# Optimization experiments

Hardware: AMD Instinct MI355X
Metric: run time of the kernel (lower is better)

## Reference

```python
import jax, jax.numpy as jnp
import numpy as np

N = 50000      # num nodes
NE = 20000     # num hyperedges
NNZ = 1000000  # incidence pairs |{(v,e)}|
F_IN = 128
HID = 64
NCLS = 40
NLAYER = 4
ALPHA = 0.1    # args.restart_alpha
LAMDA = 0.5


def setup_inputs() -> dict:
    key = jax.random.key(0)
    ks = jax.random.split(key, 8)
    x = jax.random.normal(ks[0], (N, F_IN), dtype=jnp.float32)
    vertex = jax.random.randint(ks[1], (NNZ,), 0, N, dtype=jnp.int32)
    edges = jax.random.randint(ks[2], (NNZ,), 0, NE, dtype=jnp.int32)
    W0 = jax.random.normal(ks[3], (F_IN, HID), dtype=jnp.float32) / np.float32(np.sqrt(F_IN))
    b0 = jnp.zeros((HID,), jnp.float32)
    Ws = jax.random.normal(ks[4], (NLAYER, HID, HID), dtype=jnp.float32) / np.float32(np.sqrt(HID))
    Wout = jax.random.normal(ks[5], (HID, NCLS), dtype=jnp.float32) / np.float32(np.sqrt(HID))
    bout = jnp.zeros((NCLS,), jnp.float32)
    return {"x": x, "vertex": vertex, "edges": edges, "W0": W0, "b0": b0,
            "Ws": Ws, "Wout": Wout, "bout": bout}


def _scatter_mean(src, idx, num_segments):
    s = jax.ops.segment_sum(src, idx, num_segments=num_segments)
    cnt = jax.ops.segment_sum(jnp.ones((idx.shape[0],), src.dtype), idx, num_segments=num_segments)
    return s / jnp.maximum(cnt, 1.0)[:, None]


def _normalize_l2(X):
    # torch: rownorm = X.detach().norm(dim=1, keepdim=True); scale = rownorm^-1; inf->0
    norm = jax.lax.stop_gradient(jnp.sqrt(jnp.sum(X * X, axis=-1, keepdims=True)))
    scale = jnp.where(norm > 0, 1.0 / jnp.maximum(norm, jnp.float32(1e-30)), 0.0)
    return X * scale


def reference(x, vertex, edges, W0, b0, Ws, Wout, bout):
    # input linear + relu (dropout = identity in eval mode)
    X = jax.nn.relu(x @ W0 + b0)
    X0 = X
    for i in range(NLAYER):
        beta = float(np.log(LAMDA / (i + 1) + 1.0))
        Xve = X[vertex]                       # gather node -> incidence  [NNZ, HID]
        Xe = _scatter_mean(Xve, edges, NE)    # scatter-mean -> hyperedge [NE, HID]
        Xev = Xe[edges]                       # gather hyperedge -> incidence [NNZ, HID]
        Xv = _scatter_mean(Xev, vertex, N)    # scatter-mean -> node      [N, HID]
        Xv = _normalize_l2(Xv)                # args.UniGNN_use_norm = True
        Xi = (1.0 - ALPHA) * Xv + ALPHA * X0
        X = jax.nn.relu((1.0 - beta) * Xi + beta * (Xi @ Ws[i]))
    return X @ Wout + bout
```

## Files before the change

### kernel.cpp

```cpp
#include <hip/hip_runtime.h>
#include <hip/hip_fp16.h>
#include <math.h>

#define N_NODES 50000
#define N_EDGES 20000
#define NNZ_C   1000000
#define F_IN    128
#define HID     64
#define NCLS    40
#define NLAYER  4
#define ALPHA   0.1f

#define ESHIFT  6
#define VSHIFT  7
#define NB_E    ((N_EDGES + 63) / 64)
#define NB_V    ((N_NODES + 127) / 128)
#define NB_TOT  (NB_E + NB_V)
#define MAXNB   391

typedef _Float16 f16x8 __attribute__((ext_vector_type(8)));
typedef float    f32x4 __attribute__((ext_vector_type(4)));

__global__ __launch_bounds__(256) void input_gemm(
    const float* __restrict__ x, const float* __restrict__ W0,
    const float* __restrict__ b0, _Float16* __restrict__ X0h,
    _Float16* __restrict__ Xh)
{
    int lane = threadIdx.x & 63;
    int wv   = threadIdx.x >> 6;
    int r16  = lane & 15;
    int kgrp = lane >> 4;
    f16x8 bf[4][4];
    #pragma unroll
    for (int n0 = 0; n0 < 4; ++n0)
        #pragma unroll
        for (int kh = 0; kh < 4; ++kh)
            #pragma unroll
            for (int j = 0; j < 8; ++j)
                bf[n0][kh][j] = (_Float16)W0[(kh * 32 + kgrp * 8 + j) * HID + n0 * 16 + r16];
    float bias[4];
    #pragma unroll
    for (int n0 = 0; n0 < 4; ++n0) bias[n0] = b0[n0 * 16 + r16];

    int nwaves = gridDim.x * 4;
    for (int t = blockIdx.x * 4 + wv; t < N_NODES / 16; t += nwaves) {
        int row0 = t * 16;
        const float* xp = x + (size_t)(row0 + r16) * F_IN + kgrp * 8;
        f16x8 a[4];
        #pragma unroll
        for (int kh = 0; kh < 4; ++kh) {
            float4 u0 = *(const float4*)(xp + kh * 32);
            float4 u1 = *(const float4*)(xp + kh * 32 + 4);
            a[kh][0] = (_Float16)u0.x; a[kh][1] = (_Float16)u0.y;
            a[kh][2] = (_Float16)u0.z; a[kh][3] = (_Float16)u0.w;
            a[kh][4] = (_Float16)u1.x; a[kh][5] = (_Float16)u1.y;
            a[kh][6] = (_Float16)u1.z; a[kh][7] = (_Float16)u1.w;
        }
        #pragma unroll
        for (int n0 = 0; n0 < 4; ++n0) {
            f32x4 acc = {0.f, 0.f, 0.f, 0.f};
            #pragma unroll
            for (int kh = 0; kh < 4; ++kh)
                acc = __builtin_amdgcn_mfma_f32_16x16x32_f16(a[kh], bf[n0][kh], acc, 0, 0, 0);
            #pragma unroll
            for (int r = 0; r < 4; ++r) {
                float y = acc[r] + bias[n0];
                y = y > 0.f ? y : 0.f;
                _Float16 h = (_Float16)y;
                size_t o = (size_t)(row0 + kgrp * 4 + r) * HID + n0 * 16 + r16;
                X0h[o] = h;
                Xh[o]  = h;
            }
        }
    }
}

__global__ __launch_bounds__(256) void make_wp(
    const float* __restrict__ Ws, _Float16* __restrict__ Wp,
    float be0, float be1, float be2, float be3)
{
    int l = blockIdx.x;
    float beta = (l == 0) ? be0 : (l == 1) ? be1 : (l == 2) ? be2 : be3;
    for (int i = threadIdx.x; i < HID * HID; i += 256) {
        int k = i >> 6, n = i & 63;
        float v = beta * Ws[l * HID * HID + i] + ((k == n) ? (1.f - beta) : 0.f);
        Wp[l * HID * HID + i] = (_Float16)v;
    }
}

__global__ __launch_bounds__(256) void bucket_hist(
    const int* __restrict__ vertex, const int* __restrict__ edges,
    int* __restrict__ gcnt)
{
    __shared__ int h[NB_TOT];
    int tid = threadIdx.x;
    for (int i = tid; i < NB_TOT; i += 256) h[i] = 0;
    __syncthreads();
    int base = blockIdx.x * 4096;
    int n = NNZ_C - base; if (n > 4096) n = 4096;
    for (int i = tid * 4; i < n; i += 1024) {
        int4 e4 = *(const int4*)(edges  + base + i);
        int4 v4 = *(const int4*)(vertex + base + i);
        atomicAdd(&h[e4.x >> ESHIFT], 1);
        atomicAdd(&h[e4.y >> ESHIFT], 1);
        atomicAdd(&h[e4.z >> ESHIFT], 1);
        atomicAdd(&h[e4.w >> ESHIFT], 1);
        atomicAdd(&h[NB_E + (v4.x >> VSHIFT)], 1);
        atomicAdd(&h[NB_E + (v4.y >> VSHIFT)], 1);
        atomicAdd(&h[NB_E + (v4.z >> VSHIFT)], 1);
        atomicAdd(&h[NB_E + (v4.w >> VSHIFT)], 1);
    }
    __syncthreads();
    for (int i = tid; i < NB_TOT; i += 256)
        if (h[i]) atomicAdd(&gcnt[i], h[i]);
}

__global__ __launch_bounds__(1024) void bucket_scan(
    const int* __restrict__ gcnt, int* __restrict__ boff_e,
    int* __restrict__ boff_v, int* __restrict__ curb)
{
    __shared__ int tmp[1024];
    int tid = threadIdx.x;
    int v = (tid < NB_TOT) ? gcnt[tid] : 0;
    tmp[tid] = v;
    __syncthreads();
    for (int d = 1; d < 1024; d <<= 1) {
        int t = (tid >= d) ? tmp[tid - d] : 0;
        __syncthreads();
        tmp[tid] += t;
        __syncthreads();
    }
    if (tid < NB_TOT) {
        int excl = tmp[tid] - v;
        int off = (tid < NB_E) ? excl : excl - NNZ_C;
        if (tid < NB_E) boff_e[tid] = off; else boff_v[tid - NB_E] = off;
        curb[tid] = off;
    }
    if (tid == 0) { boff_e[NB_E] = NNZ_C; boff_v[NB_V] = NNZ_C; }
}

__global__ __launch_bounds__(256) void bin_pass1(
    const int* __restrict__ keys, const int* __restrict__ vals,
    int shift, int nb, int* __restrict__ cur,
    unsigned long long* __restrict__ binned)
{
    __shared__ int hist[MAXNB];
    __shared__ int base[MAXNB];
    int tid = threadIdx.x;
    int blk = blockIdx.x * 4096;
    int nh = NNZ_C - blk; if (nh > 4096) nh = 4096;
    for (int i = tid; i < nb; i += 256) hist[i] = 0;
    __syncthreads();
    for (int i = tid; i < nh; i += 256)
        atomicAdd(&hist[keys[blk + i] >> shift], 1);
    __syncthreads();
    for (int i = tid; i < nb; i += 256) {
        int c = hist[i];
        base[i] = c ? atomicAdd(&cur[i], c) : 0;
        hist[i] = 0;
    }
    __syncthreads();
    for (int i = tid; i < nh; i += 256) {
        int k = keys[blk + i], v = vals[blk + i];
        int bkt = k >> shift;
        int r = atomicAdd(&hist[bkt], 1);
        binned[base[bkt] + r] = ((unsigned long long)(unsigned)k << 32) | (unsigned)v;
    }
}

__global__ __launch_bounds__(256) void bin_pass2f(
    const unsigned long long* __restrict__ binned, const int* __restrict__ boff,
    int shift, int nkeys, int* __restrict__ off, float* __restrict__ inv,
    int* __restrict__ adj)
{
    __shared__ int lcnt[128];
    __shared__ int ts[128];
    __shared__ int lcur[128];
    int b  = blockIdx.x;
    int k0 = b << shift;
    int bs = 1 << shift;
    int kn = nkeys - k0; if (kn > bs) kn = bs;
    int tid = threadIdx.x;
    if (tid < 128) lcnt[tid] = 0;
    __syncthreads();
    int beg = boff[b], end = boff[b + 1];
    for (int j = beg + tid; j < end; j += 256)
        atomicAdd(&lcnt[(int)(binned[j] >> 32) - k0], 1);
    __syncthreads();
    int c = 0;
    if (tid < 128) { c = lcnt[tid]; ts[tid] = c; }
    __syncthreads();
    #pragma unroll
    for (int d = 1; d < 128; d <<= 1) {
        int t = 0;
        if (tid < 128 && tid >= d) t = ts[tid - d];
        __syncthreads();
        if (tid < 128) ts[tid] += t;
        __syncthreads();
    }
    if (tid < kn) {
        int pos = beg + ts[tid] - c;
        off[k0 + tid] = pos;
        inv[k0 + tid] = 1.0f / fmaxf((float)c, 1.0f);
        lcur[tid] = pos;
    }
    if (b == 0 && tid == 0) off[nkeys] = NNZ_C;
    __syncthreads();
    for (int j = beg + tid; j < end; j += 256) {
        unsigned long long p = binned[j];
        int k = (int)(p >> 32) - k0;
        int v = (int)(p & 0xffffffffULL);
        adj[atomicAdd(&lcur[k], 1)] = v;
    }
}

__device__ __forceinline__ void gather_rows(
    const __half* __restrict__ src, const int* __restrict__ adj,
    int beg, int end, int lane, float acc[8])
{
    int g = lane >> 3, c = lane & 7;
    for (int j = beg; j < end; j += 64) {
        int nj = end - j; if (nj > 64) nj = 64;
        int myidx = (lane < nj) ? adj[j + lane] : 0;
        for (int s = 0; (s << 3) < nj; ++s) {
            int r = (s << 3) + g;
            int srcl = r < nj ? r : 0;
            int idx = __shfl(myidx, srcl);
            if (r < nj) {
                uint4 raw = ((const uint4*)(src + (size_t)idx * HID))[c];
                union { uint4 u; __half2 h[4]; } U; U.u = raw;
                float2 f0 = __half22float2(U.h[0]);
                float2 f1 = __half22float2(U.h[1]);
                float2 f2 = __half22float2(U.h[2]);
                float2 f3 = __half22float2(U.h[3]);
                acc[0] += f0.x; acc[1] += f0.y;
                acc[2] += f1.x; acc[3] += f1.y;
                acc[4] += f2.x; acc[5] += f2.y;
                acc[6] += f3.x; acc[7] += f3.y;
            }
        }
    }
    #pragma unroll
    for (int q = 0; q < 8; ++q) {
        acc[q] += __shfl_xor(acc[q], 8);
        acc[q] += __shfl_xor(acc[q], 16);
        acc[q] += __shfl_xor(acc[q], 32);
    }
}

__global__ __launch_bounds__(256) void edge_gather(
    const __half* __restrict__ Xh, const int* __restrict__ adj_e,
    const int* __restrict__ off_e, const float* __restrict__ inv_e,
    __half* __restrict__ Xeh)
{
    int wid  = blockIdx.x * 4 + (threadIdx.x >> 6);
    int lane = threadIdx.x & 63;
    float acc[8] = {0.f,0.f,0.f,0.f,0.f,0.f,0.f,0.f};
    gather_rows(Xh, adj_e, off_e[wid], off_e[wid + 1], lane, acc);
    if ((lane >> 3) == 0) {
        float sc = inv_e[wid];
        union { uint4 u; __half2 h[4]; } O;
        O.h[0] = __floats2half2_rn(acc[0] * sc, acc[1] * sc);
        O.h[1] = __floats2half2_rn(acc[2] * sc, acc[3] * sc);
        O.h[2] = __floats2half2_rn(acc[4] * sc, acc[5] * sc);
        O.h[3] = __floats2half2_rn(acc[6] * sc, acc[7] * sc);
        ((uint4*)(Xeh + (size_t)wid * HID))[lane] = O.u;
    }
}

__global__ __launch_bounds__(256) void node_gather(
    const __half* __restrict__ Xeh, const int* __restrict__ adj_v,
    const int* __restrict__ off_v, const float* __restrict__ inv_v,
    const _Float16* __restrict__ X0h, _Float16* __restrict__ Xi)
{
    int wv   = threadIdx.x >> 6;
    int row  = blockIdx.x * 4 + wv;
    int lane = threadIdx.x & 63;
    float acc[8] = {0.f,0.f,0.f,0.f,0.f,0.f,0.f,0.f};
    gather_rows(Xeh, adj_v, off_v[row], off_v[row + 1], lane, acc);
    float scm = inv_v[row];
    float m[8]; float s = 0.f;
    #pragma unroll
    for (int q = 0; q < 8; ++q) { m[q] = acc[q] * scm; s += m[q] * m[q]; }
    s += __shfl_xor(s, 1);
    s += __shfl_xor(s, 2);
    s += __shfl_xor(s, 4);
    float norm  = sqrtf(s);
    float scale = norm > 0.f ? 1.0f / norm : 0.f;
    if ((lane >> 3) == 0) {
        union { f16x8 v; uint4 u; } I;
        I.u = *(const uint4*)(X0h + (size_t)row * HID + lane * 8);
        union { f16x8 v; uint4 u; } O;
        #pragma unroll
        for (int q = 0; q < 8; ++q)
            O.v[q] = (_Float16)((1.0f - ALPHA) * (m[q] * scale) + ALPHA * (float)I.v[q]);
        *(uint4*)(Xi + (size_t)row * HID + lane * 8) = O.u;
    }
}

__global__ __launch_bounds__(256) void layer_gemm(
    const _Float16* __restrict__ Xi, const _Float16* __restrict__ Wp,
    _Float16* __restrict__ Xh)
{
    int lane = threadIdx.x & 63;
    int wv   = threadIdx.x >> 6;
    int r16  = lane & 15;
    int kgrp = lane >> 4;
    f16x8 bf[4][2];
    #pragma unroll
    for (int n0 = 0; n0 < 4; ++n0)
        #pragma unroll
        for (int kh = 0; kh < 2; ++kh) {
            #pragma unroll
            for (int j = 0; j < 8; ++j)
                bf[n0][kh][j] = Wp[(kh * 32 + kgrp * 8 + j) * HID + n0 * 16 + r16];
        }
    int nwaves = gridDim.x * 4;
    for (int t = blockIdx.x * 4 + wv; t < N_NODES / 16; t += nwaves) {
        int row0 = t * 16;
        const _Float16* ap = Xi + (size_t)(row0 + r16) * HID + kgrp * 8;
        f16x8 a0 = *(const f16x8*)(ap);
        f16x8 a1 = *(const f16x8*)(ap + 32);
        #pragma unroll
        for (int n0 = 0; n0 < 4; ++n0) {
            f32x4 acc = {0.f, 0.f, 0.f, 0.f};
            acc = __builtin_amdgcn_mfma_f32_16x16x32_f16(a0, bf[n0][0], acc, 0, 0, 0);
            acc = __builtin_amdgcn_mfma_f32_16x16x32_f16(a1, bf[n0][1], acc, 0, 0, 0);
            #pragma unroll
            for (int r = 0; r < 4; ++r) {
                float y = acc[r] > 0.f ? acc[r] : 0.f;
                Xh[(size_t)(row0 + kgrp * 4 + r) * HID + n0 * 16 + r16] = (_Float16)y;
            }
        }
    }
}

__global__ __launch_bounds__(256) void out_gemm(
    const _Float16* __restrict__ Xh, const float* __restrict__ Wout,
    const float* __restrict__ bout, float* __restrict__ out)
{
    int lane = threadIdx.x & 63;
    int wv   = threadIdx.x >> 6;
    int r16  = lane & 15;
    int kgrp = lane >> 4;
    f16x8 bf[3][2];
    float bias[3];
    #pragma unroll
    for (int n0 = 0; n0 < 3; ++n0) {
        int col = n0 * 16 + r16;
        bias[n0] = (col < NCLS) ? bout[col] : 0.f;
        #pragma unroll
        for (int kh = 0; kh < 2; ++kh)
            #pragma unroll
            for (int j = 0; j < 8; ++j) {
                int k = kh * 32 + kgrp * 8 + j;
                bf[n0][kh][j] = (col < NCLS) ? (_Float16)Wout[k * NCLS + col] : (_Float16)0.f;
            }
    }
    int nwaves = gridDim.x * 4;
    for (int t = blockIdx.x * 4 + wv; t < N_NODES / 16; t += nwaves) {
        int row0 = t * 16;
        const _Float16* ap = Xh + (size_t)(row0 + r16) * HID + kgrp * 8;
        f16x8 a0 = *(const f16x8*)(ap);
        f16x8 a1 = *(const f16x8*)(ap + 32);
        #pragma unroll
        for (int n0 = 0; n0 < 3; ++n0) {
            f32x4 acc = {0.f, 0.f, 0.f, 0.f};
            acc = __builtin_amdgcn_mfma_f32_16x16x32_f16(a0, bf[n0][0], acc, 0, 0, 0);
            acc = __builtin_amdgcn_mfma_f32_16x16x32_f16(a1, bf[n0][1], acc, 0, 0, 0);
            int col = n0 * 16 + r16;
            if (col < NCLS) {
                #pragma unroll
                for (int r = 0; r < 4; ++r)
                    out[(size_t)(row0 + kgrp * 4 + r) * NCLS + col] = acc[r] + bias[n0];
            }
        }
    }
}

extern "C" void kernel_launch(void* const* d_in, const int* in_sizes, int n_in,
                              void* d_out, int out_size, void* d_ws, size_t ws_size,
                              hipStream_t stream)
{
    const float* x      = (const float*)d_in[0];
    const int*   vertex = (const int*)  d_in[1];
    const int*   edges  = (const int*)  d_in[2];
    const float* W0     = (const float*)d_in[3];
    const float* b0     = (const float*)d_in[4];
    const float* Ws     = (const float*)d_in[5];
    const float* Wout   = (const float*)d_in[6];
    const float* bout   = (const float*)d_in[7];
    float* out = (float*)d_out;

    char* ws = (char*)d_ws;
    unsigned long long* binned = (unsigned long long*)ws; ws += (size_t)NNZ_C * 8;
    _Float16*  X0h  = (_Float16*)ws;  ws += (size_t)N_NODES * HID * 2;
    _Float16*  Xh   = (_Float16*)ws;  ws += (size_t)N_NODES * HID * 2;
    _Float16*  Xi   = (_Float16*)ws;  ws += (size_t)N_NODES * HID * 2;
    __half*    Xeh  = (__half*)ws;    ws += (size_t)N_EDGES * HID * 2;
    _Float16*  Wp   = (_Float16*)ws;  ws += (size_t)NLAYER * HID * HID * 2;
    int*   adj_e  = (int*)ws;     ws += (size_t)NNZ_C * 4;
    int*   adj_v  = (int*)ws;     ws += (size_t)NNZ_C * 4;
    int*   off_e  = (int*)ws;     ws += (size_t)(N_EDGES + 1) * 4;
    int*   off_v  = (int*)ws;     ws += (size_t)(N_NODES + 1) * 4;
    float* inv_e  = (float*)ws;   ws += (size_t)N_EDGES * 4;
    float* inv_v  = (float*)ws;   ws += (size_t)N_NODES * 4;
    int*   gcnt   = (int*)ws;     ws += (size_t)NB_TOT * 4;
    int*   boff_e = (int*)ws;     ws += (size_t)(NB_E + 1) * 4;
    int*   boff_v = (int*)ws;     ws += (size_t)(NB_V + 1) * 4;
    int*   curb   = (int*)ws;     ws += (size_t)NB_TOT * 4;

    const int p1_grid = (NNZ_C + 4095) / 4096;

    hipMemsetAsync(gcnt, 0, (size_t)NB_TOT * 4, stream);
    bucket_hist<<<p1_grid, 256, 0, stream>>>(vertex, edges, gcnt);
    bucket_scan<<<1, 1024, 0, stream>>>(gcnt, boff_e, boff_v, curb);

    bin_pass1<<<p1_grid, 256, 0, stream>>>(edges, vertex, ESHIFT, NB_E, curb, binned);
    bin_pass2f<<<NB_E, 256, 0, stream>>>(binned, boff_e, ESHIFT, N_EDGES, off_e, inv_e, adj_e);
    bin_pass1<<<p1_grid, 256, 0, stream>>>(vertex, edges, VSHIFT, NB_V, curb + NB_E, binned);
    bin_pass2f<<<NB_V, 256, 0, stream>>>(binned, boff_v, VSHIFT, N_NODES, off_v, inv_v, adj_v);

    float be0 = logf(0.5f / 1.f + 1.0f);
    float be1 = logf(0.5f / 2.f + 1.0f);
    float be2 = logf(0.5f / 3.f + 1.0f);
    float be3 = logf(0.5f / 4.f + 1.0f);
    make_wp<<<NLAYER, 256, 0, stream>>>(Ws, Wp, be0, be1, be2, be3);

    input_gemm<<<391, 256, 0, stream>>>(x, W0, b0, X0h, Xh);

    for (int l = 0; l < NLAYER; ++l) {
        edge_gather<<<N_EDGES / 4, 256, 0, stream>>>((__half*)Xh, adj_e, off_e, inv_e, Xeh);
        node_gather<<<N_NODES / 4, 256, 0, stream>>>(
            Xeh, adj_v, off_v, inv_v, X0h, Xi);
        layer_gemm<<<391, 256, 0, stream>>>(Xi, Wp + (size_t)l * HID * HID, Xh);
    }

    out_gemm<<<391, 256, 0, stream>>>(Xh, Wout, bout, out);
}
```

Baseline: 293.4 us.

## Map one segment per 8-lane group in gathers and fuse both binning passes

The edge and node gather kernels now give each group of 8 lanes its own segment instead of one segment per wavefront. Each group loops up to the wave's maximum degree, loading indices directly with no shuffle broadcast and no cross-group reduction. Edges have about 50 incidences and nodes about 20, so the old mapping left many lanes idle and paid reduction overhead. The two bin_pass1 launches are merged into one kernel that reads vertex/edges once and writes two binned buffers, at the cost of an extra 8 MB of workspace. Degree imbalance within a wave can now cause lanes to sit idle.

```diff
diff --git a/kernel.cpp b/kernel.cpp
--- a/kernel.cpp
+++ b/kernel.cpp
@@ -16,7 +16,6 @@
 #define NB_E    ((N_EDGES + 63) / 64)
 #define NB_V    ((N_NODES + 127) / 128)
 #define NB_TOT  (NB_E + NB_V)
-#define MAXNB   391
 
 typedef _Float16 f16x8 __attribute__((ext_vector_type(8)));
 typedef float    f32x4 __attribute__((ext_vector_type(4)));
@@ -139,32 +138,38 @@
     if (tid == 0) { boff_e[NB_E] = NNZ_C; boff_v[NB_V] = NNZ_C; }
 }
 
-__global__ __launch_bounds__(256) void bin_pass1(
-    const int* __restrict__ keys, const int* __restrict__ vals,
-    int shift, int nb, int* __restrict__ cur,
-    unsigned long long* __restrict__ binned)
-{
-    __shared__ int hist[MAXNB];
-    __shared__ int base[MAXNB];
+__global__ __launch_bounds__(256) void bin_pass1_both(
+    const int* __restrict__ vertex, const int* __restrict__ edges,
+    int* __restrict__ curb,
+    unsigned long long* __restrict__ binned_e,
+    unsigned long long* __restrict__ binned_v)
+{
+    __shared__ int hist[NB_TOT];
+    __shared__ int base[NB_TOT];
     int tid = threadIdx.x;
     int blk = blockIdx.x * 4096;
     int nh = NNZ_C - blk; if (nh > 4096) nh = 4096;
-    for (int i = tid; i < nb; i += 256) hist[i] = 0;
-    __syncthreads();
-    for (int i = tid; i < nh; i += 256)
-        atomicAdd(&hist[keys[blk + i] >> shift], 1);
-    __syncthreads();
-    for (int i = tid; i < nb; i += 256) {
+    for (int i = tid; i < NB_TOT; i += 256) hist[i] = 0;
+    __syncthreads();
+    for (int i = tid; i < nh; i += 256) {
+        atomicAdd(&hist[edges[blk + i] >> ESHIFT], 1);
+        atomicAdd(&hist[NB_E + (vertex[blk + i] >> VSHIFT)], 1);
+    }
+    __syncthreads();
+    for (int i = tid; i < NB_TOT; i += 256) {
         int c = hist[i];
-        base[i] = c ? atomicAdd(&cur[i], c) : 0;
+        base[i] = c ? atomicAdd(&curb[i], c) : 0;
         hist[i] = 0;
     }
     __syncthreads();
     for (int i = tid; i < nh; i += 256) {
-        int k = keys[blk + i], v = vals[blk + i];
-        int bkt = k >> shift;
-        int r = atomicAdd(&hist[bkt], 1);
-        binned[base[bkt] + r] = ((unsigned long long)(unsigned)k << 32) | (unsigned)v;
+        int e = edges[blk + i], v = vertex[blk + i];
+        int be = e >> ESHIFT;
+        int r  = atomicAdd(&hist[be], 1);
+        binned_e[base[be] + r] = ((unsigned long long)(unsigned)e << 32) | (unsigned)v;
+        int bv = NB_E + (v >> VSHIFT);
+        int r2 = atomicAdd(&hist[bv], 1);
+        binned_v[base[bv] + r2] = ((unsigned long long)(unsigned)v << 32) | (unsigned)e;
     }
 }
 
@@ -214,38 +219,34 @@
     }
 }
 
-__device__ __forceinline__ void gather_rows(
+__device__ __forceinline__ void gather_seg8(
     const __half* __restrict__ src, const int* __restrict__ adj,
-    int beg, int end, int lane, float acc[8])
-{
-    int g = lane >> 3, c = lane & 7;
-    for (int j = beg; j < end; j += 64) {
-        int nj = end - j; if (nj > 64) nj = 64;
-        int myidx = (lane < nj) ? adj[j + lane] : 0;
-        for (int s = 0; (s << 3) < nj; ++s) {
-            int r = (s << 3) + g;
-            int srcl = r < nj ? r : 0;
-            int idx = __shfl(myidx, srcl);
-            if (r < nj) {
-                uint4 raw = ((const uint4*)(src + (size_t)idx * HID))[c];
-                union { uint4 u; __half2 h[4]; } U; U.u = raw;
-                float2 f0 = __half22float2(U.h[0]);
-                float2 f1 = __half22float2(U.h[1]);
-                float2 f2 = __half22float2(U.h[2]);
-                float2 f3 = __half22float2(U.h[3]);
-                acc[0] += f0.x; acc[1] += f0.y;
-                acc[2] += f1.x; acc[3] += f1.y;
-                acc[4] += f2.x; acc[5] += f2.y;
-                acc[6] += f3.x; acc[7] += f3.y;
-            }
-        }
-    }
-    #pragma unroll
-    for (int q = 0; q < 8; ++q) {
-        acc[q] += __shfl_xor(acc[q], 8);
-        acc[q] += __shfl_xor(acc[q], 16);
-        acc[q] += __shfl_xor(acc[q], 32);
-    }
+    int beg, int deg, int md, int c, float acc[8])
+{
+    for (int t = 0; t < md; ++t) {
+        if (t < deg) {
+            int idx = adj[beg + t];
+            uint4 raw = ((const uint4*)(src + (size_t)idx * HID))[c];
+            union { uint4 u; __half2 h[4]; } U; U.u = raw;
+            float2 f0 = __half22float2(U.h[0]);
+            float2 f1 = __half22float2(U.h[1]);
+            float2 f2 = __half22float2(U.h[2]);
+            float2 f3 = __half22float2(U.h[3]);
+            acc[0] += f0.x; acc[1] += f0.y;
+            acc[2] += f1.x; acc[3] += f1.y;
+            acc[4] += f2.x; acc[5] += f2.y;
+            acc[6] += f3.x; acc[7] += f3.y;
+        }
+    }
+}
+
+__device__ __forceinline__ int wave_max_deg(int deg)
+{
+    int md = deg;
+    md = max(md, __shfl_xor(md, 8));
+    md = max(md, __shfl_xor(md, 16));
+    md = max(md, __shfl_xor(md, 32));
+    return md;
 }
 
 __global__ __launch_bounds__(256) void edge_gather(
@@ -255,17 +256,20 @@
 {
     int wid  = blockIdx.x * 4 + (threadIdx.x >> 6);
     int lane = threadIdx.x & 63;
+    int g = lane >> 3, c = lane & 7;
+    int e = wid * 8 + g;
+    int beg = off_e[e];
+    int deg = off_e[e + 1] - beg;
+    int md  = wave_max_deg(deg);
     float acc[8] = {0.f,0.f,0.f,0.f,0.f,0.f,0.f,0.f};
-    gather_rows(Xh, adj_e, off_e[wid], off_e[wid + 1], lane, acc);
-    if ((lane >> 3) == 0) {
-        float sc = inv_e[wid];
-        union { uint4 u; __half2 h[4]; } O;
-        O.h[0] = __floats2half2_rn(acc[0] * sc, acc[1] * sc);
-        O.h[1] = __floats2half2_rn(acc[2] * sc, acc[3] * sc);
-        O.h[2] = __floats2half2_rn(acc[4] * sc, acc[5] * sc);
-        O.h[3] = __floats2half2_rn(acc[6] * sc, acc[7] * sc);
-        ((uint4*)(Xeh + (size_t)wid * HID))[lane] = O.u;
-    }
+    gather_seg8(Xh, adj_e, beg, deg, md, c, acc);
+    float sc = inv_e[e];
+    union { uint4 u; __half2 h[4]; } O;
+    O.h[0] = __floats2half2_rn(acc[0] * sc, acc[1] * sc);
+    O.h[1] = __floats2half2_rn(acc[2] * sc, acc[3] * sc);
+    O.h[2] = __floats2half2_rn(acc[4] * sc, acc[5] * sc);
+    O.h[3] = __floats2half2_rn(acc[6] * sc, acc[7] * sc);
+    *(uint4*)(Xeh + (size_t)e * HID + c * 8) = O.u;
 }
 
 __global__ __launch_bounds__(256) void node_gather(
@@ -273,28 +277,33 @@
     const int* __restrict__ off_v, const float* __restrict__ inv_v,
     const _Float16* __restrict__ X0h, _Float16* __restrict__ Xi)
 {
-    int wv   = threadIdx.x >> 6;
-    int row  = blockIdx.x * 4 + wv;
+    int wid  = blockIdx.x * 4 + (threadIdx.x >> 6);
     int lane = threadIdx.x & 63;
+    int g = lane >> 3, c = lane & 7;
+    int v = wid * 8 + g;
+    bool ok = v < N_NODES;
+    int beg = 0, deg = 0;
+    if (ok) { beg = off_v[v]; deg = off_v[v + 1] - beg; }
+    int md = wave_max_deg(deg);
     float acc[8] = {0.f,0.f,0.f,0.f,0.f,0.f,0.f,0.f};
-    gather_rows(Xeh, adj_v, off_v[row], off_v[row + 1], lane, acc);
-    float scm = inv_v[row];
-    float m[8]; float s = 0.f;
-    #pragma unroll
-    for (int q = 0; q < 8; ++q) { m[q] = acc[q] * scm; s += m[q] * m[q]; }
-    s += __shfl_xor(s, 1);
-    s += __shfl_xor(s, 2);
-    s += __shfl_xor(s, 4);
-    float norm  = sqrtf(s);
-    float scale = norm > 0.f ? 1.0f / norm : 0.f;
-    if ((lane >> 3) == 0) {
-        union { f16x8 v; uint4 u; } I;
-        I.u = *(const uint4*)(X0h + (size_t)row * HID + lane * 8);
-        union { f16x8 v; uint4 u; } O;
+    gather_seg8(Xeh, adj_v, beg, deg, md, c, acc);
+    if (ok) {
+        float scm = inv_v[v];
+        float m[8]; float s = 0.f;
+        #pragma unroll
+        for (int q = 0; q < 8; ++q) { m[q] = acc[q] * scm; s += m[q] * m[q]; }
+        s += __shfl_xor(s, 1);
+        s += __shfl_xor(s, 2);
+        s += __shfl_xor(s, 4);
+        float norm  = sqrtf(s);
+        float scale = norm > 0.f ? 1.0f / norm : 0.f;
+        union { f16x8 vv; uint4 u; } I;
+        I.u = *(const uint4*)(X0h + (size_t)v * HID + c * 8);
+        union { f16x8 vv; uint4 u; } O;
         #pragma unroll
         for (int q = 0; q < 8; ++q)
-            O.v[q] = (_Float16)((1.0f - ALPHA) * (m[q] * scale) + ALPHA * (float)I.v[q]);
-        *(uint4*)(Xi + (size_t)row * HID + lane * 8) = O.u;
+            O.vv[q] = (_Float16)((1.0f - ALPHA) * (m[q] * scale) + ALPHA * (float)I.vv[q]);
+        *(uint4*)(Xi + (size_t)v * HID + c * 8) = O.u;
     }
 }
 
@@ -393,7 +402,8 @@
     float* out = (float*)d_out;
 
     char* ws = (char*)d_ws;
-    unsigned long long* binned = (unsigned long long*)ws; ws += (size_t)NNZ_C * 8;
+    unsigned long long* binned_e = (unsigned long long*)ws; ws += (size_t)NNZ_C * 8;
+    unsigned long long* binned_v = (unsigned long long*)ws; ws += (size_t)NNZ_C * 8;
     _Float16*  X0h  = (_Float16*)ws;  ws += (size_t)N_NODES * HID * 2;
     _Float16*  Xh   = (_Float16*)ws;  ws += (size_t)N_NODES * HID * 2;
     _Float16*  Xi   = (_Float16*)ws;  ws += (size_t)N_NODES * HID * 2;
@@ -415,11 +425,9 @@
     hipMemsetAsync(gcnt, 0, (size_t)NB_TOT * 4, stream);
     bucket_hist<<<p1_grid, 256, 0, stream>>>(vertex, edges, gcnt);
     bucket_scan<<<1, 1024, 0, stream>>>(gcnt, boff_e, boff_v, curb);
-
-    bin_pass1<<<p1_grid, 256, 0, stream>>>(edges, vertex, ESHIFT, NB_E, curb, binned);
-    bin_pass2f<<<NB_E, 256, 0, stream>>>(binned, boff_e, ESHIFT, N_EDGES, off_e, inv_e, adj_e);
-    bin_pass1<<<p1_grid, 256, 0, stream>>>(vertex, edges, VSHIFT, NB_V, curb + NB_E, binned);
-    bin_pass2f<<<NB_V, 256, 0, stream>>>(binned, boff_v, VSHIFT, N_NODES, off_v, inv_v, adj_v);
+    bin_pass1_both<<<p1_grid, 256, 0, stream>>>(vertex, edges, curb, binned_e, binned_v);
+    bin_pass2f<<<NB_E, 256, 0, stream>>>(binned_e, boff_e, ESHIFT, N_EDGES, off_e, inv_e, adj_e);
+    bin_pass2f<<<NB_V, 256, 0, stream>>>(binned_v, boff_v, VSHIFT, N_NODES, off_v, inv_v, adj_v);
 
     float be0 = logf(0.5f / 1.f + 1.0f);
     float be1 = logf(0.5f / 2.f + 1.0f);
@@ -430,8 +438,8 @@
     input_gemm<<<391, 256, 0, stream>>>(x, W0, b0, X0h, Xh);
 
     for (int l = 0; l < NLAYER; ++l) {
-        edge_gather<<<N_EDGES / 4, 256, 0, stream>>>((__half*)Xh, adj_e, off_e, inv_e, Xeh);
-        node_gather<<<N_NODES / 4, 256, 0, stream>>>(
+        edge_gather<<<N_EDGES / 8 / 4, 256, 0, stream>>>((__half*)Xh, adj_e, off_e, inv_e, Xeh);
+        node_gather<<<(N_NODES / 8 + 3) / 4, 256, 0, stream>>>(
             Xeh, adj_v, off_v, inv_v, X0h, Xi);
         layer_gemm<<<391, 256, 0, stream>>>(Xi, Wp + (size_t)l * HID * HID, Xh);
     }
```

Measured after the change: 394.8 us. 1.35x slower.

## Fuse both binning passes and pack key/value pairs into 32-bit words

Applied to the files above, without the earlier changes.

Merges the two first-pass binning kernels into one launch that reads vertex and edges once and histograms both bucket sets together. Incidence pairs are packed into 32-bit words instead of 64-bit, relying on the known index ranges, which halves the binned buffer traffic. The gather loop also hoists all eight index shuffles ahead of the loads to allow more memory-level parallelism. The packing only works because node and edge counts fit in 16 and 15 bits.

```diff
diff --git a/kernel.cpp b/kernel.cpp
--- a/kernel.cpp
+++ b/kernel.cpp
@@ -16,7 +16,6 @@
 #define NB_E    ((N_EDGES + 63) / 64)
 #define NB_V    ((N_NODES + 127) / 128)
 #define NB_TOT  (NB_E + NB_V)
-#define MAXNB   391
 
 typedef _Float16 f16x8 __attribute__((ext_vector_type(8)));
 typedef float    f32x4 __attribute__((ext_vector_type(4)));
@@ -139,39 +138,45 @@
     if (tid == 0) { boff_e[NB_E] = NNZ_C; boff_v[NB_V] = NNZ_C; }
 }
 
-__global__ __launch_bounds__(256) void bin_pass1(
-    const int* __restrict__ keys, const int* __restrict__ vals,
-    int shift, int nb, int* __restrict__ cur,
-    unsigned long long* __restrict__ binned)
-{
-    __shared__ int hist[MAXNB];
-    __shared__ int base[MAXNB];
+__global__ __launch_bounds__(256) void bin_pass1_both(
+    const int* __restrict__ vertex, const int* __restrict__ edges,
+    int* __restrict__ curb,
+    unsigned* __restrict__ binned_e,
+    unsigned* __restrict__ binned_v)
+{
+    __shared__ int hist[NB_TOT];
+    __shared__ int base[NB_TOT];
     int tid = threadIdx.x;
     int blk = blockIdx.x * 4096;
     int nh = NNZ_C - blk; if (nh > 4096) nh = 4096;
-    for (int i = tid; i < nb; i += 256) hist[i] = 0;
-    __syncthreads();
-    for (int i = tid; i < nh; i += 256)
-        atomicAdd(&hist[keys[blk + i] >> shift], 1);
-    __syncthreads();
-    for (int i = tid; i < nb; i += 256) {
+    for (int i = tid; i < NB_TOT; i += 256) hist[i] = 0;
+    __syncthreads();
+    for (int i = tid; i < nh; i += 256) {
+        atomicAdd(&hist[edges[blk + i] >> ESHIFT], 1);
+        atomicAdd(&hist[NB_E + (vertex[blk + i] >> VSHIFT)], 1);
+    }
+    __syncthreads();
+    for (int i = tid; i < NB_TOT; i += 256) {
         int c = hist[i];
-        base[i] = c ? atomicAdd(&cur[i], c) : 0;
+        base[i] = c ? atomicAdd(&curb[i], c) : 0;
         hist[i] = 0;
     }
     __syncthreads();
     for (int i = tid; i < nh; i += 256) {
-        int k = keys[blk + i], v = vals[blk + i];
-        int bkt = k >> shift;
-        int r = atomicAdd(&hist[bkt], 1);
-        binned[base[bkt] + r] = ((unsigned long long)(unsigned)k << 32) | (unsigned)v;
+        int e = edges[blk + i], v = vertex[blk + i];
+        int be = e >> ESHIFT;
+        int r  = atomicAdd(&hist[be], 1);
+        binned_e[base[be] + r] = ((unsigned)e << 16) | (unsigned)v;
+        int bv = NB_E + (v >> VSHIFT);
+        int r2 = atomicAdd(&hist[bv], 1);
+        binned_v[base[bv] + r2] = ((unsigned)v << 15) | (unsigned)e;
     }
 }
 
 __global__ __launch_bounds__(256) void bin_pass2f(
-    const unsigned long long* __restrict__ binned, const int* __restrict__ boff,
-    int shift, int nkeys, int* __restrict__ off, float* __restrict__ inv,
-    int* __restrict__ adj)
+    const unsigned* __restrict__ binned, const int* __restrict__ boff,
+    int shift, int kshift, int nkeys,
+    int* __restrict__ off, float* __restrict__ inv, int* __restrict__ adj)
 {
     __shared__ int lcnt[128];
     __shared__ int ts[128];
@@ -181,11 +186,12 @@
     int bs = 1 << shift;
     int kn = nkeys - k0; if (kn > bs) kn = bs;
     int tid = threadIdx.x;
+    unsigned vmask = (1u << kshift) - 1u;
     if (tid < 128) lcnt[tid] = 0;
     __syncthreads();
     int beg = boff[b], end = boff[b + 1];
     for (int j = beg + tid; j < end; j += 256)
-        atomicAdd(&lcnt[(int)(binned[j] >> 32) - k0], 1);
+        atomicAdd(&lcnt[(int)(binned[j] >> kshift) - k0], 1);
     __syncthreads();
     int c = 0;
     if (tid < 128) { c = lcnt[tid]; ts[tid] = c; }
@@ -207,9 +213,9 @@
     if (b == 0 && tid == 0) off[nkeys] = NNZ_C;
     __syncthreads();
     for (int j = beg + tid; j < end; j += 256) {
-        unsigned long long p = binned[j];
-        int k = (int)(p >> 32) - k0;
-        int v = (int)(p & 0xffffffffULL);
+        unsigned p = binned[j];
+        int k = (int)(p >> kshift) - k0;
+        int v = (int)(p & vmask);
         adj[atomicAdd(&lcur[k], 1)] = v;
     }
 }
@@ -222,12 +228,15 @@
     for (int j = beg; j < end; j += 64) {
         int nj = end - j; if (nj > 64) nj = 64;
         int myidx = (lane < nj) ? adj[j + lane] : 0;
-        for (int s = 0; (s << 3) < nj; ++s) {
+        int idx[8];
+        #pragma unroll
+        for (int s = 0; s < 8; ++s)
+            idx[s] = __shfl(myidx, ((s << 3) + g) & 63);
+        #pragma unroll
+        for (int s = 0; s < 8; ++s) {
             int r = (s << 3) + g;
-            int srcl = r < nj ? r : 0;
-            int idx = __shfl(myidx, srcl);
             if (r < nj) {
-                uint4 raw = ((const uint4*)(src + (size_t)idx * HID))[c];
+                uint4 raw = ((const uint4*)(src + (size_t)idx[s] * HID))[c];
                 union { uint4 u; __half2 h[4]; } U; U.u = raw;
                 float2 f0 = __half22float2(U.h[0]);
                 float2 f1 = __half22float2(U.h[1]);
@@ -393,7 +402,8 @@
     float* out = (float*)d_out;
 
     char* ws = (char*)d_ws;
-    unsigned long long* binned = (unsigned long long*)ws; ws += (size_t)NNZ_C * 8;
+    unsigned* binned_e = (unsigned*)ws; ws += (size_t)NNZ_C * 4;
+    unsigned* binned_v = (unsigned*)ws; ws += (size_t)NNZ_C * 4;
     _Float16*  X0h  = (_Float16*)ws;  ws += (size_t)N_NODES * HID * 2;
     _Float16*  Xh   = (_Float16*)ws;  ws += (size_t)N_NODES * HID * 2;
     _Float16*  Xi   = (_Float16*)ws;  ws += (size_t)N_NODES * HID * 2;
@@ -415,11 +425,9 @@
     hipMemsetAsync(gcnt, 0, (size_t)NB_TOT * 4, stream);
     bucket_hist<<<p1_grid, 256, 0, stream>>>(vertex, edges, gcnt);
     bucket_scan<<<1, 1024, 0, stream>>>(gcnt, boff_e, boff_v, curb);
-
-    bin_pass1<<<p1_grid, 256, 0, stream>>>(edges, vertex, ESHIFT, NB_E, curb, binned);
-    bin_pass2f<<<NB_E, 256, 0, stream>>>(binned, boff_e, ESHIFT, N_EDGES, off_e, inv_e, adj_e);
-    bin_pass1<<<p1_grid, 256, 0, stream>>>(vertex, edges, VSHIFT, NB_V, curb + NB_E, binned);
-    bin_pass2f<<<NB_V, 256, 0, stream>>>(binned, boff_v, VSHIFT, N_NODES, off_v, inv_v, adj_v);
+    bin_pass1_both<<<p1_grid, 256, 0, stream>>>(vertex, edges, curb, binned_e, binned_v);
+    bin_pass2f<<<NB_E, 256, 0, stream>>>(binned_e, boff_e, ESHIFT, 16, N_EDGES, off_e, inv_e, adj_e);
+    bin_pass2f<<<NB_V, 256, 0, stream>>>(binned_v, boff_v, VSHIFT, 15, N_NODES, off_v, inv_v, adj_v);
 
     float be0 = logf(0.5f / 1.f + 1.0f);
     float be1 = logf(0.5f / 2.f + 1.0f);
```

New measurement: 285.7 us. 2.6% less time.
